# Kernel optimization log

Measured on AMD Instinct MI355X. Metric: run time of the kernel, lower is better.

Reference implementation:

```python
import jax, jax.numpy as jnp
import numpy as np
import math

B, S, H = 512, 100, 1024
A, N = 128, 8
TAU = 1.0


def make_pe(seq_len, hidden):
    # PositionalEncoding buffer: pe[s, 0::2]=sin(pos*div), pe[s,1::2]=cos(pos*div)
    pos = jnp.arange(seq_len, dtype=jnp.float32)[:, None]          # [S,1]
    div = jnp.exp(jnp.arange(0, hidden, 2, dtype=jnp.float32) * (-math.log(10000.0) / hidden))
    pe = jnp.zeros((seq_len, hidden), dtype=jnp.float32)
    pe = pe.at[:, 0::2].set(jnp.sin(pos * div))
    pe = pe.at[:, 1::2].set(jnp.cos(pos * div))
    return pe                                                      # [S,H]


def setup_inputs() -> dict:
    key = jax.random.key(0)
    kx, kq, kk, kg = jax.random.split(key, 4)
    x = jax.random.normal(kx, (B, S, H), dtype=jnp.float32)
    # torch Linear weight layout: [out_features, in_features]
    Wq = jax.random.normal(kq, (A * N, H), dtype=jnp.float32) * (1.0 / math.sqrt(H))
    Wk = jax.random.normal(kk, (A * N, H), dtype=jnp.float32) * (1.0 / math.sqrt(H))
    # pre-sampled standard Gumbel noise (deterministic reference)
    u = jax.random.uniform(kg, (B * N, S), dtype=jnp.float32, minval=1e-6, maxval=1.0 - 1e-6)
    gumbel = -jnp.log(-jnp.log(u))
    return {"x": x, "Wq": Wq, "Wk": Wk, "gumbel": gumbel}


def reference(x, Wq, Wk, gumbel):
    b, s, h = x.shape
    pos_emb = x + make_pe(s, h)[None]                              # [B,S,H]
    Q = (pos_emb @ Wq.T).reshape(b, s, N, A).transpose(0, 2, 1, 3)  # [B,N,S,A]
    K = (pos_emb @ Wk.T).reshape(b, s, N, A).transpose(0, 2, 1, 3)  # [B,N,S,A]
    # original: sum_t (Q . K_t) / sqrt(H) / S  ==  Q . (sum_t K_t) / (sqrt(H)*S)
    Ksum = K.sum(axis=2)                                           # [B,N,A]
    logits = jnp.einsum('bnsa,bna->bns', Q, Ksum) / (math.sqrt(h) * s)
    y = (logits.reshape(b * N, s) + gumbel) / TAU
    soft = jax.nn.softmax(y, axis=-1)
    hard = jax.nn.one_hot(jnp.argmax(y, axis=-1), s, dtype=soft.dtype)
    # straight-through (forward value == hard one-hot)
    alphas = (hard - jax.lax.stop_gradient(soft) + soft).reshape(b, N, s)
    out = jnp.einsum('bns,bsh->bnh', alphas, x)                    # gather selected timesteps
    return out
```

## Files before the change

kernel.cpp:

```cpp
#include <hip/hip_runtime.h>
#include <float.h>
#include <math.h>

#define Bc 512
#define Sc 100
#define Hc 1024
#define Ac 128
#define Nc 8
#define PDST 196

__global__ __launch_bounds__(256) void pe_kernel(float* __restrict__ pe){
  int s = blockIdx.x;
  int t = threadIdx.x;
  const float fac = (float)(-9.210340371976184 / 1024.0);
  for(int i = t; i < Hc/2; i += 256){
    float div = expf((float)(2*i) * fac);
    float a = (float)s * div;
    pe[s*Hc + 2*i]     = sinf(a);
    pe[s*Hc + 2*i + 1] = cosf(a);
  }
}

__global__ __launch_bounds__(256) void pesum_kernel(const float* __restrict__ pe, float* __restrict__ pesum){
  int h = blockIdx.x*256 + threadIdx.x;
  float acc = 0.f;
  for(int s = 0; s < Sc; ++s) acc += pe[s*Hc + h];
  pesum[h] = acc;
}

__global__ __launch_bounds__(256) void xsum_kernel(const float* __restrict__ x, const float* __restrict__ pesum,
                                                   float* __restrict__ xsp){
  int b = blockIdx.x;
  int q = blockIdx.y;
  int t = threadIdx.x;
  const float4* xr = (const float4*)(x + (size_t)b*Sc*Hc);
  float4 acc;
  if(q == 0) acc = ((const float4*)pesum)[t];
  else       acc = make_float4(0.f,0.f,0.f,0.f);
  int s0 = q*25;
  #pragma unroll 5
  for(int s = s0; s < s0+25; ++s){
    float4 v = xr[s*(Hc/4) + t];
    acc.x += v.x; acc.y += v.y; acc.z += v.z; acc.w += v.w;
  }
  ((float4*)(xsp + ((size_t)b*4 + q)*Hc))[t] = acc;
}

__global__ __launch_bounds__(256) void xsred_kernel(const float* __restrict__ xsp, float* __restrict__ xs){
  int b = blockIdx.x, t = threadIdx.x;
  const float4* p = (const float4*)(xsp + (size_t)b*4*Hc);
  float4 a = p[t], b1 = p[256+t], c = p[512+t], d = p[768+t];
  a.x += b1.x + c.x + d.x;
  a.y += b1.y + c.y + d.y;
  a.z += b1.z + c.z + d.z;
  a.w += b1.w + c.w + d.w;
  ((float4*)(xs + (size_t)b*Hc))[t] = a;
}

__global__ __launch_bounds__(256) void ksum_gemm4(const float* __restrict__ xs, const float* __restrict__ Wk,
                                                  float* __restrict__ Ksum8){
  __shared__ float As[32*PDST];
  __shared__ float Bs[32*PDST];
  const int t = threadIdx.x;
  const int j0 = blockIdx.x*128, b0 = blockIdx.y*128, kb = blockIdx.z*128;
  const int ty = t>>4, tx = t&15;
  const int lr = t>>1, lh = t&1;
  const int pj = (lr>>3)*12 + (lr&7);

  float acc[8][8];
  #pragma unroll
  for(int i = 0; i < 8; ++i)
    #pragma unroll
    for(int j = 0; j < 8; ++j) acc[i][j] = 0.f;

  const float* xa = xs + (size_t)(b0+lr)*Hc + kb + lh*16;
  const float* wa = Wk + (size_t)(j0+lr)*Hc + kb + lh*16;
  float4 a4[4], b4[4], a4n[4], b4n[4];
  #pragma unroll
  for(int i = 0; i < 4; ++i){ a4[i] = *(const float4*)(xa + i*4);
                              b4[i] = *(const float4*)(wa + i*4); }

  for(int c0 = 0; c0 < 4; ++c0){
    __syncthreads();
    #pragma unroll
    for(int i = 0; i < 4; ++i){
      int k = lh*16 + i*4;
      As[(k+0)*PDST + pj] = a4[i].x; As[(k+1)*PDST + pj] = a4[i].y;
      As[(k+2)*PDST + pj] = a4[i].z; As[(k+3)*PDST + pj] = a4[i].w;
      Bs[(k+0)*PDST + pj] = b4[i].x; Bs[(k+1)*PDST + pj] = b4[i].y;
      Bs[(k+2)*PDST + pj] = b4[i].z; Bs[(k+3)*PDST + pj] = b4[i].w;
    }
    if(c0 < 3){
      #pragma unroll
      for(int i = 0; i < 4; ++i){
        a4n[i] = *(const float4*)(xa + (c0+1)*32 + i*4);
        b4n[i] = *(const float4*)(wa + (c0+1)*32 + i*4);
      }
    }
    __syncthreads();
    #pragma unroll 4
    for(int kk = 0; kk < 32; ++kk){
      const float* ar = &As[kk*PDST + ty*12];
      const float* br = &Bs[kk*PDST + tx*12];
      float4 au = *(const float4*)(ar),   av = *(const float4*)(ar + 4);
      float4 bu = *(const float4*)(br),   bv = *(const float4*)(br + 4);
      float am[8] = {au.x,au.y,au.z,au.w, av.x,av.y,av.z,av.w};
      float bn[8] = {bu.x,bu.y,bu.z,bu.w, bv.x,bv.y,bv.z,bv.w};
      #pragma unroll
      for(int i = 0; i < 8; ++i)
        #pragma unroll
        for(int j = 0; j < 8; ++j)
          acc[i][j] = fmaf(am[i], bn[j], acc[i][j]);
    }
    a4[0]=a4n[0]; a4[1]=a4n[1]; a4[2]=a4n[2]; a4[3]=a4n[3];
    b4[0]=b4n[0]; b4[1]=b4n[1]; b4[2]=b4n[2]; b4[3]=b4n[3];
  }

  #pragma unroll
  for(int i = 0; i < 8; ++i){
    float* cp = Ksum8 + (((size_t)blockIdx.z*Bc + b0 + ty*8 + i)<<10) + j0 + tx*8;
    *(float4*)cp     = make_float4(acc[i][0],acc[i][1],acc[i][2],acc[i][3]);
    *(float4*)(cp+4) = make_float4(acc[i][4],acc[i][5],acc[i][6],acc[i][7]);
  }
}

__global__ __launch_bounds__(256) void ksred8_kernel(const float* __restrict__ Ksum8, float* __restrict__ Ksum){
  int b = blockIdx.x, t = threadIdx.x;
  const float4* p = (const float4*)(Ksum8 + ((size_t)b<<10));
  const size_t sl = (size_t)Bc*Hc/4;
  float4 a = p[t];
  #pragma unroll
  for(int i = 1; i < 8; ++i){
    float4 q = p[i*sl + t];
    a.x += q.x; a.y += q.y; a.z += q.z; a.w += q.w;
  }
  ((float4*)(Ksum + ((size_t)b<<10)))[t] = a;
}

__global__ __launch_bounds__(256) void v_gemm4(const float* __restrict__ Ksum, const float* __restrict__ Wq,
                                               float* __restrict__ v){
  __shared__ float As[32*PDST];
  __shared__ float Bs[32*PDST];
  const int t = threadIdx.x;
  const int h0 = blockIdx.x*128, b0 = blockIdx.y*128, n = blockIdx.z;
  const int ty = t>>4, tx = t&15;
  const int lr = t>>1, lh = t&1;
  const int pj = (lr>>3)*12 + (lr&7);
  const int rr = t>>3, cc = t&7;

  float acc[8][8];
  #pragma unroll
  for(int i = 0; i < 8; ++i)
    #pragma unroll
    for(int j = 0; j < 8; ++j) acc[i][j] = 0.f;

  const float* ka = Ksum + (size_t)(b0+lr)*Hc + n*Ac + lh*16;
  float4 a4[4], b4[4], a4n[4], b4n[4];
  #pragma unroll
  for(int i = 0; i < 4; ++i){
    a4[i] = *(const float4*)(ka + i*4);
    b4[i] = *(const float4*)(Wq + (size_t)(n*Ac + rr)*Hc + h0 + cc*16 + i*4);
  }

  for(int c0 = 0; c0 < 4; ++c0){
    __syncthreads();
    #pragma unroll
    for(int i = 0; i < 4; ++i){
      int k = lh*16 + i*4;
      As[(k+0)*PDST + pj] = a4[i].x; As[(k+1)*PDST + pj] = a4[i].y;
      As[(k+2)*PDST + pj] = a4[i].z; As[(k+3)*PDST + pj] = a4[i].w;
      int h = cc*16 + i*4;
      *(float4*)&Bs[rr*PDST + (h>>3)*12 + (h&7)] = b4[i];
    }
    if(c0 < 3){
      #pragma unroll
      for(int i = 0; i < 4; ++i){
        a4n[i] = *(const float4*)(ka + (c0+1)*32 + i*4);
        b4n[i] = *(const float4*)(Wq + (size_t)(n*Ac + (c0+1)*32 + rr)*Hc + h0 + cc*16 + i*4);
      }
    }
    __syncthreads();
    #pragma unroll 4
    for(int kk = 0; kk < 32; ++kk){
      const float* ar = &As[kk*PDST + ty*12];
      const float* br = &Bs[kk*PDST + tx*12];
      float4 au = *(const float4*)(ar),   av = *(const float4*)(ar + 4);
      float4 bu = *(const float4*)(br),   bv = *(const float4*)(br + 4);
      float am[8] = {au.x,au.y,au.z,au.w, av.x,av.y,av.z,av.w};
      float bn[8] = {bu.x,bu.y,bu.z,bu.w, bv.x,bv.y,bv.z,bv.w};
      #pragma unroll
      for(int i = 0; i < 8; ++i)
        #pragma unroll
        for(int j = 0; j < 8; ++j)
          acc[i][j] = fmaf(am[i], bn[j], acc[i][j]);
    }
    a4[0]=a4n[0]; a4[1]=a4n[1]; a4[2]=a4n[2]; a4[3]=a4n[3];
    b4[0]=b4n[0]; b4[1]=b4n[1]; b4[2]=b4n[2]; b4[3]=b4n[3];
  }

  #pragma unroll
  for(int i = 0; i < 8; ++i){
    float* cp = v + (((size_t)(b0 + ty*8 + i)*Nc + n)<<10) + h0 + tx*8;
    *(float4*)cp     = make_float4(acc[i][0],acc[i][1],acc[i][2],acc[i][3]);
    *(float4*)(cp+4) = make_float4(acc[i][4],acc[i][5],acc[i][6],acc[i][7]);
  }
}

__global__ __launch_bounds__(512) void attn_kernel(const float* __restrict__ x, const float* __restrict__ pe,
                                                   const float* __restrict__ v, const float* __restrict__ g,
                                                   float* __restrict__ out){
  __shared__ float4 tile[1600];
  __shared__ float part[8][Nc][104];
  __shared__ int sidx[Nc];
  const int b = blockIdx.x;
  const int t = threadIdx.x;
  const int lane = t & 63;
  const int kq = __builtin_amdgcn_readfirstlane(t >> 6);

  const int rA = t >> 4,          cA = t & 15;
  const int rB = (t+512) >> 4,    cB = (t+512) & 15;
  const int rC = (t+1024) >> 4,   cC = (t+1024) & 15;
  const bool hasD = (t < 64);
  const int rD = (t+1536) >> 4,   cD = (t+1536) & 15;

  const float* xb = x + (size_t)b*Sc*Hc;
  const float* vb = v + (size_t)b*Nc*Hc;

  const int r0 = lane;
  const int r1v = lane + 64;
  const int r1 = (r1v < Sc) ? r1v : (Sc-1);
  const bool val1 = (r1v < Sc);

  float acc0[Nc], acc1[Nc];
  #pragma unroll
  for(int n = 0; n < Nc; ++n){ acc0[n] = 0.f; acc1[n] = 0.f; }

  float4 xvA = *(const float4*)(xb + rA*Hc + cA*4);
  float4 pvA = *(const float4*)(pe + rA*Hc + cA*4);
  float4 xvB = *(const float4*)(xb + rB*Hc + cB*4);
  float4 pvB = *(const float4*)(pe + rB*Hc + cB*4);
  float4 xvC = *(const float4*)(xb + rC*Hc + cC*4);
  float4 pvC = *(const float4*)(pe + rC*Hc + cC*4);
  float4 xvD = make_float4(0,0,0,0), pvD = make_float4(0,0,0,0);
  if(hasD){ xvD = *(const float4*)(xb + rD*Hc + cD*4);
            pvD = *(const float4*)(pe + rD*Hc + cD*4); }

  for(int kt = 0; kt < 16; ++kt){
    __syncthreads();
    tile[rA*16 + (cA ^ (rA&7))] = make_float4(xvA.x+pvA.x, xvA.y+pvA.y, xvA.z+pvA.z, xvA.w+pvA.w);
    tile[rB*16 + (cB ^ (rB&7))] = make_float4(xvB.x+pvB.x, xvB.y+pvB.y, xvB.z+pvB.z, xvB.w+pvB.w);
    tile[rC*16 + (cC ^ (rC&7))] = make_float4(xvC.x+pvC.x, xvC.y+pvC.y, xvC.z+pvC.z, xvC.w+pvC.w);
    if(hasD)
      tile[rD*16 + (cD ^ (rD&7))] = make_float4(xvD.x+pvD.x, xvD.y+pvD.y, xvD.z+pvD.z, xvD.w+pvD.w);
    if(kt < 15){
      int ko = (kt+1)*64;
      xvA = *(const float4*)(xb + rA*Hc + ko + cA*4);
      pvA = *(const float4*)(pe + rA*Hc + ko + cA*4);
      xvB = *(const float4*)(xb + rB*Hc + ko + cB*4);
      pvB = *(const float4*)(pe + rB*Hc + ko + cB*4);
      xvC = *(const float4*)(xb + rC*Hc + ko + cC*4);
      pvC = *(const float4*)(pe + rC*Hc + ko + cC*4);
      if(hasD){ xvD = *(const float4*)(xb + rD*Hc + ko + cD*4);
                pvD = *(const float4*)(pe + rD*Hc + ko + cD*4); }
    }
    __syncthreads();
    #pragma unroll
    for(int j = 0; j < 2; ++j){
      float4 xe0 = tile[r0*16 + ((kq*2 + j) ^ (r0&7))];
      float4 xe1 = tile[r1*16 + ((kq*2 + j) ^ (r1&7))];
      const float* vk = vb + kt*64 + kq*8 + j*4;
      #pragma unroll
      for(int n = 0; n < Nc; ++n){
        float4 vv = *(const float4*)(vk + n*Hc);
        acc0[n] = fmaf(xe0.x, vv.x, acc0[n]);
        acc0[n] = fmaf(xe0.y, vv.y, acc0[n]);
        acc0[n] = fmaf(xe0.z, vv.z, acc0[n]);
        acc0[n] = fmaf(xe0.w, vv.w, acc0[n]);
        acc1[n] = fmaf(xe1.x, vv.x, acc1[n]);
        acc1[n] = fmaf(xe1.y, vv.y, acc1[n]);
        acc1[n] = fmaf(xe1.z, vv.z, acc1[n]);
        acc1[n] = fmaf(xe1.w, vv.w, acc1[n]);
      }
    }
  }
  #pragma unroll
  for(int n = 0; n < Nc; ++n){
    part[kq][n][r0] = acc0[n];
    if(val1) part[kq][n][r1v] = acc1[n];
  }
  __syncthreads();

  {
    int n = kq, j = lane;
    float best = -FLT_MAX; int bidx = 0;
    #pragma unroll
    for(int i = 0; i < 2; ++i){
      int s2 = j + 64*i;
      if(s2 < Sc){
        float dot = 0.f;
        #pragma unroll
        for(int q = 0; q < 8; ++q) dot += part[q][n][s2];
        float y = dot/3200.0f + g[(size_t)(b*Nc + n)*Sc + s2];
        if(y > best){ best = y; bidx = s2; }
      }
    }
    #pragma unroll
    for(int m = 32; m >= 1; m >>= 1){
      float ob = __shfl_xor(best, m, 64);
      int   oi = __shfl_xor(bidx, m, 64);
      if(ob > best || (ob == best && oi < bidx)){ best = ob; bidx = oi; }
    }
    if(j == 0) sidx[n] = bidx;
  }
  __syncthreads();

  const float4* xb4 = (const float4*)xb;
  float4* ob4 = (float4*)(out + (size_t)b*Nc*Hc);
  #pragma unroll
  for(int i = 0; i < 4; ++i){
    int idx = i*512 + t;
    int nn = idx >> 8, c = idx & 255;
    ob4[idx] = xb4[sidx[nn]*256 + c];
  }
}

extern "C" void kernel_launch(void* const* d_in, const int* in_sizes, int n_in,
                              void* d_out, int out_size, void* d_ws, size_t ws_size,
                              hipStream_t stream) {
  const float* x  = (const float*)d_in[0];
  const float* Wq = (const float*)d_in[1];
  const float* Wk = (const float*)d_in[2];
  const float* g  = (const float*)d_in[3];
  float* out = (float*)d_out;

  char* ws = (char*)d_ws;
  float* pe    = (float*)(ws);
  float* pesum = (float*)(ws +    409600);
  float* xsp   = (float*)(ws +    413696);
  float* xs    = (float*)(ws +   8802304);
  float* Ksum8 = (float*)(ws +  10899456);
  float* Ksum  = (float*)(ws +  27676672);
  float* v     = (float*)(ws +    413696);

  pe_kernel    <<<100, 256, 0, stream>>>(pe);
  pesum_kernel <<<4,   256, 0, stream>>>(pe, pesum);
  xsum_kernel  <<<dim3(512,4), 256, 0, stream>>>(x, pesum, xsp);
  xsred_kernel <<<512, 256, 0, stream>>>(xsp, xs);
  ksum_gemm4   <<<dim3(8,4,8), 256, 0, stream>>>(xs, Wk, Ksum8);
  ksred8_kernel<<<512, 256, 0, stream>>>(Ksum8, Ksum);
  v_gemm4      <<<dim3(8,4,8), 256, 0, stream>>>(Ksum, Wq, v);
  attn_kernel  <<<512, 512, 0, stream>>>(x, pe, v, g, out);
}
```

Before: 144.5 us.

## Split attention logits over two K halves and add separate argmax-gather kernel

The fused attention kernel is split in two. A logits kernel runs on a 512x2 grid, where each block covers half of the hidden dimension, uses a smaller shared tile and writes partial logits to the workspace. A new amax kernel sums the two partials, adds the Gumbel noise, takes the argmax and gathers the selected rows of x. The goal is more blocks and lower LDS use per block, for better occupancy and load balance across CUs. The cost is an extra kernel launch and a partial-logit round trip through global memory.

New measurement: 150.0 us. 3.8% more time.

```diff
diff --git a/kernel.cpp b/kernel.cpp
--- a/kernel.cpp
+++ b/kernel.cpp
@@ -206,100 +206,109 @@
   }
 }
 
-__global__ __launch_bounds__(512) void attn_kernel(const float* __restrict__ x, const float* __restrict__ pe,
-                                                   const float* __restrict__ v, const float* __restrict__ g,
-                                                   float* __restrict__ out){
-  __shared__ float4 tile[1600];
+__global__ __launch_bounds__(512) void logits_kernel(const float* __restrict__ x, const float* __restrict__ pe,
+                                                     const float* __restrict__ v, float* __restrict__ lgp){
+  __shared__ float4 tile[800];
   __shared__ float part[8][Nc][104];
+  const int b = blockIdx.x;
+  const int kh = blockIdx.y;
+  const int t = threadIdx.x;
+  const int lane = t & 63;
+  const int kq = __builtin_amdgcn_readfirstlane(t >> 6);
+
+  const int rA = t >> 3,  cA = t & 7;
+  const bool hasB = (t < 288);
+  const int eB = t + 512;
+  const int rB = eB >> 3, cB = eB & 7;
+
+  const float* xb = x + (size_t)b*Sc*Hc;
+  const float* vb = v + (size_t)b*Nc*Hc + kh*512;
+  const int kbase = kh*128;
+
+  const int r0 = lane;
+  const int r1v = lane + 64;
+  const int r1 = (r1v < Sc) ? r1v : (Sc-1);
+  const bool val1 = (r1v < Sc);
+
+  float acc0[Nc], acc1[Nc];
+  #pragma unroll
+  for(int n = 0; n < Nc; ++n){ acc0[n] = 0.f; acc1[n] = 0.f; }
+
+  float4 xvA = ((const float4*)xb)[rA*256 + kbase + cA];
+  float4 pvA = ((const float4*)pe)[rA*256 + kbase + cA];
+  float4 xvB = make_float4(0,0,0,0), pvB = make_float4(0,0,0,0);
+  if(hasB){ xvB = ((const float4*)xb)[rB*256 + kbase + cB];
+            pvB = ((const float4*)pe)[rB*256 + kbase + cB]; }
+
+  for(int kt = 0; kt < 16; ++kt){
+    __syncthreads();
+    tile[rA*8 + (cA ^ (rA&7))] = make_float4(xvA.x+pvA.x, xvA.y+pvA.y, xvA.z+pvA.z, xvA.w+pvA.w);
+    if(hasB)
+      tile[rB*8 + (cB ^ (rB&7))] = make_float4(xvB.x+pvB.x, xvB.y+pvB.y, xvB.z+pvB.z, xvB.w+pvB.w);
+    if(kt < 15){
+      int ko = kbase + (kt+1)*8;
+      xvA = ((const float4*)xb)[rA*256 + ko + cA];
+      pvA = ((const float4*)pe)[rA*256 + ko + cA];
+      if(hasB){ xvB = ((const float4*)xb)[rB*256 + ko + cB];
+                pvB = ((const float4*)pe)[rB*256 + ko + cB]; }
+    }
+    __syncthreads();
+    float4 xe0 = tile[r0*8 + (kq ^ (r0&7))];
+    float4 xe1 = tile[r1*8 + (kq ^ (r1&7))];
+    const float* vk = vb + kt*32 + kq*4;
+    #pragma unroll
+    for(int n = 0; n < Nc; ++n){
+      float4 vv = *(const float4*)(vk + n*Hc);
+      acc0[n] = fmaf(xe0.x, vv.x, acc0[n]);
+      acc0[n] = fmaf(xe0.y, vv.y, acc0[n]);
+      acc0[n] = fmaf(xe0.z, vv.z, acc0[n]);
+      acc0[n] = fmaf(xe0.w, vv.w, acc0[n]);
+      acc1[n] = fmaf(xe1.x, vv.x, acc1[n]);
+      acc1[n] = fmaf(xe1.y, vv.y, acc1[n]);
+      acc1[n] = fmaf(xe1.z, vv.z, acc1[n]);
+      acc1[n] = fmaf(xe1.w, vv.w, acc1[n]);
+    }
+  }
+  #pragma unroll
+  for(int n = 0; n < Nc; ++n){
+    part[kq][n][r0] = acc0[n];
+    if(val1) part[kq][n][r1v] = acc1[n];
+  }
+  __syncthreads();
+
+  {
+    int n = kq;
+    #pragma unroll
+    for(int i = 0; i < 2; ++i){
+      int s2 = lane + 64*i;
+      if(s2 < Sc){
+        float dot = 0.f;
+        #pragma unroll
+        for(int q = 0; q < 8; ++q) dot += part[q][n][s2];
+        lgp[((size_t)(kh*Bc + b)*Nc + n)*104 + s2] = dot;
+      }
+    }
+  }
+}
+
+__global__ __launch_bounds__(256) void amax_kernel(const float* __restrict__ x, const float* __restrict__ lgp,
+                                                   const float* __restrict__ g, float* __restrict__ out){
   __shared__ int sidx[Nc];
   const int b = blockIdx.x;
   const int t = threadIdx.x;
   const int lane = t & 63;
-  const int kq = __builtin_amdgcn_readfirstlane(t >> 6);
-
-  const int rA = t >> 4,          cA = t & 15;
-  const int rB = (t+512) >> 4,    cB = (t+512) & 15;
-  const int rC = (t+1024) >> 4,   cC = (t+1024) & 15;
-  const bool hasD = (t < 64);
-  const int rD = (t+1536) >> 4,   cD = (t+1536) & 15;
-
-  const float* xb = x + (size_t)b*Sc*Hc;
-  const float* vb = v + (size_t)b*Nc*Hc;
-
-  const int r0 = lane;
-  const int r1v = lane + 64;
-  const int r1 = (r1v < Sc) ? r1v : (Sc-1);
-  const bool val1 = (r1v < Sc);
-
-  float acc0[Nc], acc1[Nc];
-  #pragma unroll
-  for(int n = 0; n < Nc; ++n){ acc0[n] = 0.f; acc1[n] = 0.f; }
-
-  float4 xvA = *(const float4*)(xb + rA*Hc + cA*4);
-  float4 pvA = *(const float4*)(pe + rA*Hc + cA*4);
-  float4 xvB = *(const float4*)(xb + rB*Hc + cB*4);
-  float4 pvB = *(const float4*)(pe + rB*Hc + cB*4);
-  float4 xvC = *(const float4*)(xb + rC*Hc + cC*4);
-  float4 pvC = *(const float4*)(pe + rC*Hc + cC*4);
-  float4 xvD = make_float4(0,0,0,0), pvD = make_float4(0,0,0,0);
-  if(hasD){ xvD = *(const float4*)(xb + rD*Hc + cD*4);
-            pvD = *(const float4*)(pe + rD*Hc + cD*4); }
-
-  for(int kt = 0; kt < 16; ++kt){
-    __syncthreads();
-    tile[rA*16 + (cA ^ (rA&7))] = make_float4(xvA.x+pvA.x, xvA.y+pvA.y, xvA.z+pvA.z, xvA.w+pvA.w);
-    tile[rB*16 + (cB ^ (rB&7))] = make_float4(xvB.x+pvB.x, xvB.y+pvB.y, xvB.z+pvB.z, xvB.w+pvB.w);
-    tile[rC*16 + (cC ^ (rC&7))] = make_float4(xvC.x+pvC.x, xvC.y+pvC.y, xvC.z+pvC.z, xvC.w+pvC.w);
-    if(hasD)
-      tile[rD*16 + (cD ^ (rD&7))] = make_float4(xvD.x+pvD.x, xvD.y+pvD.y, xvD.z+pvD.z, xvD.w+pvD.w);
-    if(kt < 15){
-      int ko = (kt+1)*64;
-      xvA = *(const float4*)(xb + rA*Hc + ko + cA*4);
-      pvA = *(const float4*)(pe + rA*Hc + ko + cA*4);
-      xvB = *(const float4*)(xb + rB*Hc + ko + cB*4);
-      pvB = *(const float4*)(pe + rB*Hc + ko + cB*4);
-      xvC = *(const float4*)(xb + rC*Hc + ko + cC*4);
-      pvC = *(const float4*)(pe + rC*Hc + ko + cC*4);
-      if(hasD){ xvD = *(const float4*)(xb + rD*Hc + ko + cD*4);
-                pvD = *(const float4*)(pe + rD*Hc + ko + cD*4); }
-    }
-    __syncthreads();
-    #pragma unroll
-    for(int j = 0; j < 2; ++j){
-      float4 xe0 = tile[r0*16 + ((kq*2 + j) ^ (r0&7))];
-      float4 xe1 = tile[r1*16 + ((kq*2 + j) ^ (r1&7))];
-      const float* vk = vb + kt*64 + kq*8 + j*4;
-      #pragma unroll
-      for(int n = 0; n < Nc; ++n){
-        float4 vv = *(const float4*)(vk + n*Hc);
-        acc0[n] = fmaf(xe0.x, vv.x, acc0[n]);
-        acc0[n] = fmaf(xe0.y, vv.y, acc0[n]);
-        acc0[n] = fmaf(xe0.z, vv.z, acc0[n]);
-        acc0[n] = fmaf(xe0.w, vv.w, acc0[n]);
-        acc1[n] = fmaf(xe1.x, vv.x, acc1[n]);
-        acc1[n] = fmaf(xe1.y, vv.y, acc1[n]);
-        acc1[n] = fmaf(xe1.z, vv.z, acc1[n]);
-        acc1[n] = fmaf(xe1.w, vv.w, acc1[n]);
-      }
-    }
-  }
-  #pragma unroll
-  for(int n = 0; n < Nc; ++n){
-    part[kq][n][r0] = acc0[n];
-    if(val1) part[kq][n][r1v] = acc1[n];
-  }
-  __syncthreads();
-
-  {
-    int n = kq, j = lane;
+  const int w = t >> 6;
+
+  #pragma unroll
+  for(int h2 = 0; h2 < 2; ++h2){
+    int n = w + h2*4;
     float best = -FLT_MAX; int bidx = 0;
     #pragma unroll
     for(int i = 0; i < 2; ++i){
-      int s2 = j + 64*i;
+      int s2 = lane + 64*i;
       if(s2 < Sc){
-        float dot = 0.f;
-        #pragma unroll
-        for(int q = 0; q < 8; ++q) dot += part[q][n][s2];
+        float dot = lgp[((size_t)b*Nc + n)*104 + s2]
+                  + lgp[((size_t)(Bc + b)*Nc + n)*104 + s2];
         float y = dot/3200.0f + g[(size_t)(b*Nc + n)*Sc + s2];
         if(y > best){ best = y; bidx = s2; }
       }
@@ -310,15 +319,15 @@
       int   oi = __shfl_xor(bidx, m, 64);
       if(ob > best || (ob == best && oi < bidx)){ best = ob; bidx = oi; }
     }
-    if(j == 0) sidx[n] = bidx;
+    if(lane == 0) sidx[n] = bidx;
   }
   __syncthreads();
 
-  const float4* xb4 = (const float4*)xb;
+  const float4* xb4 = (const float4*)(x + (size_t)b*Sc*Hc);
   float4* ob4 = (float4*)(out + (size_t)b*Nc*Hc);
   #pragma unroll
-  for(int i = 0; i < 4; ++i){
-    int idx = i*512 + t;
+  for(int i = 0; i < 8; ++i){
+    int idx = i*256 + t;
     int nn = idx >> 8, c = idx & 255;
     ob4[idx] = xb4[sidx[nn]*256 + c];
   }
@@ -340,6 +349,7 @@
   float* xs    = (float*)(ws +   8802304);
   float* Ksum8 = (float*)(ws +  10899456);
   float* Ksum  = (float*)(ws +  27676672);
+  float* lgp   = (float*)(ws +  29773824);
   float* v     = (float*)(ws +    413696);
 
   pe_kernel    <<<100, 256, 0, stream>>>(pe);
@@ -349,5 +359,6 @@
   ksum_gemm4   <<<dim3(8,4,8), 256, 0, stream>>>(xs, Wk, Ksum8);
   ksred8_kernel<<<512, 256, 0, stream>>>(Ksum8, Ksum);
   v_gemm4      <<<dim3(8,4,8), 256, 0, stream>>>(Ksum, Wq, v);
-  attn_kernel  <<<512, 512, 0, stream>>>(x, pe, v, g, out);
-}
+  logits_kernel<<<dim3(512,2), 512, 0, stream>>>(x, pe, v, lgp);
+  amax_kernel  <<<512, 256, 0, stream>>>(x, lgp, g, out);
+}
```
